# Kernel optimization log

Measured on AMD Instinct MI355X. Metric: run time of the kernel, lower is better.

## Reference

```python
import jax, jax.numpy as jnp
import numpy as np

TEMP = 0.1
NEG = -1e30  # stands in for removing the diagonal via masked_select
EPS = 1e-12  # F.normalize eps


def _l2norm(x, axis):
    n = jnp.linalg.norm(x, axis=axis, keepdims=True)
    return x / jnp.maximum(n, EPS)


def setup_inputs() -> dict:
    key = jax.random.key(0)
    k = jax.random.split(key, 6)
    B, D = 8192, 128      # instance batch, embed dim
    Bp, P = 256, 256      # patch batch, patches per sample
    v1_ins = jax.random.normal(k[0], (B, D), jnp.float32)
    v2_ins = jax.random.normal(k[1], (B, D), jnp.float32)
    v1_patch = jax.random.normal(k[2], (Bp, D, P), jnp.float32)
    v2_patch = jax.random.normal(k[3], (Bp, D, P), jnp.float32)
    v1_counts = jax.random.randint(k[4], (Bp, P), 0, 50, dtype=jnp.int32)
    v2_counts = jax.random.randint(k[5], (Bp, P), 0, 50, dtype=jnp.int32)
    return {"v1_ins": v1_ins, "v2_ins": v2_ins,
            "v1_patch": v1_patch, "v2_patch": v2_patch,
            "v1_counts": v1_counts, "v2_counts": v2_counts}


def _instance_ce(v1, v2):
    B = v1.shape[0]
    embs = jnp.concatenate([_l2norm(v1, 1), _l2norm(v2, 1)], axis=0)  # [2B, D]
    logits = (embs @ embs.T) / TEMP                                    # [2B, 2B]
    N = 2 * B
    # masking the diagonal to -inf == masked_select removal; positive of row i
    # is column (i+B) mod 2B (matches labels after diagonal removal shift)
    logits = jnp.where(jnp.eye(N, dtype=bool), NEG, logits)
    labels = jnp.concatenate([jnp.arange(B) + B, jnp.arange(B)])
    logp = jax.nn.log_softmax(logits, axis=1)
    return -jnp.mean(logp[jnp.arange(N), labels])


def _patch_ce(v1, v2, c1, c2):
    Bp, D, P = v1.shape
    embs = jnp.concatenate([_l2norm(v1, 1), _l2norm(v2, 1)], axis=2)   # [Bp, D, 2P]
    logits = jnp.einsum('bdi,bdj->bij', embs, embs) / TEMP             # [Bp, 2P, 2P]
    N = 2 * P
    logits = jnp.where(jnp.eye(N, dtype=bool)[None], NEG, logits)
    labels = jnp.concatenate([jnp.arange(P) + P, jnp.arange(P)])       # [2P]
    valid = ~jnp.concatenate([c1 == 0, c2 == 0], axis=1)               # [Bp, 2P]
    logp = jax.nn.log_softmax(logits, axis=2)
    pos = logp[:, jnp.arange(N), labels]                               # [Bp, 2P]
    # ignore_index=-100 -> mean over non-ignored elements
    n_valid = jnp.sum(valid.astype(logits.dtype))
    return -jnp.sum(jnp.where(valid, pos, 0.0)) / n_valid


def reference(v1_ins, v2_ins, v1_patch, v2_patch, v1_counts, v2_counts):
    ins_ce = _instance_ce(v1_ins, v2_ins)
    patch_ce = _patch_ce(v1_patch, v2_patch, v1_counts, v2_counts)
    return ins_ce + patch_ce
```

## Files before the change

kernel.cpp:

```cpp
#include <hip/hip_runtime.h>
#include <math.h>

typedef __bf16 bf16_t;
typedef __bf16 bf16x8 __attribute__((ext_vector_type(8)));
typedef float f32x4 __attribute__((ext_vector_type(4)));
typedef float f32x2 __attribute__((ext_vector_type(2)));

#define B_INS 8192
#define N_INS 16384
#define D 128
#define BP 256
#define P 256
#define NP 512

#define C1_CONST 14.426950408889634f

#define WS_ACC 0
#define WS_POS 8
#define WS_PPOS (WS_POS + N_INS)
#define NPAIRI 8128
#define WS_CI (WS_PPOS + BP * NP)
#define WS_RI (WS_CI + NPAIRI * 256)
#define WS_CP (WS_RI + 1088 * 256)
#define WS_RP (WS_CP + BP * 6 * 256)
#define WS_END (WS_RP + 1024 * 256)
#define EMB_I_BYTE ((((WS_END) * 4 + 15) / 16) * 16)
#define EMB_P_BYTE (EMB_I_BYTE + N_INS * D * 2)


#define NB_NORMI 128
#define NB_NORMP 2048
#define NB_PREP (NB_NORMI + NB_NORMP + 1)
#define NB_INS 1088
#define NB_PATCHB 1024
#define NB_GRAM (NB_INS + NB_PATCHB)
#define NB_FIN (128 + 256)

__device__ __forceinline__ void load_lds16(const bf16_t* g, bf16_t* l) {
    __builtin_amdgcn_global_load_lds(
        (const __attribute__((address_space(1))) void*)g,
        (__attribute__((address_space(3))) void*)l, 16, 0, 0);
}

__device__ __forceinline__ void stage_panel(const bf16_t* __restrict__ src,
                                            bf16_t* dst, int w, int lane) {
    const bf16_t* g = src + w * 4096 + lane * 8;
    bf16_t* d = dst + w * 4096;
#pragma unroll
    for (int it = 0; it < 8; it++)
        load_lds16(g + it * 512, d + it * 512);
}

__device__ __forceinline__ void load_afrags(const bf16_t* __restrict__ abase,
                                            int rh, int tx, int q, bf16x8 af[4][4]) {
    const bf16_t* a = abase + ((rh * 64 + tx) << 3);
#pragma unroll
    for (int rt = 0; rt < 4; rt++)
#pragma unroll
        for (int ks = 0; ks < 4; ks++)
            af[rt][ks] = *(const bf16x8*)(a + (((ks << 2) + q) << 10) + (rt << 7));
}

__global__ __launch_bounds__(256) void prep_k(const float* __restrict__ v1i,
                                              const float* __restrict__ v2i,
                                              const float* __restrict__ v1p,
                                              const float* __restrict__ v2p,
                                              bf16_t* __restrict__ embI,
                                              bf16_t* __restrict__ embP,
                                              float* __restrict__ ws) {
    __shared__ float L[128][65];
    __shared__ float ps[4][64];
    __shared__ float invs[128];
    int bx = blockIdx.x;
    int t = threadIdx.x;
    if (bx < NB_NORMI) {
        int p = bx;
        const float* srcP = (p < 64) ? (v1i + (size_t)p * 128 * D)
                                     : (v2i + (size_t)(p - 64) * 128 * D);
        {
            int r = t >> 1, h = t & 1;
            const float* row = srcP + (size_t)r * D + h * 64;
            float ss = 0.f;
#pragma unroll
            for (int j = 0; j < 16; j++) {
                float4 v = *(const float4*)(row + j * 4);
                ss += v.x * v.x + v.y * v.y + v.z * v.z + v.w * v.w;
            }
            ss += __shfl_xor(ss, 1, 64);
            if (h == 0) invs[r] = 1.0f / fmaxf(sqrtf(ss), 1e-12f);
        }
        __syncthreads();
#pragma unroll
        for (int it = 0; it < 8; it++) {
            int idx = it * 256 + t;
            int r = idx & 127, g = idx >> 7;
            const float* src8 = srcP + (size_t)r * D + g * 8;
            float4 a = *(const float4*)(src8);
            float4 b = *(const float4*)(src8 + 4);
            float inv = invs[r];
            bf16x8 v;
            v[0] = (bf16_t)(a.x * inv); v[1] = (bf16_t)(a.y * inv);
            v[2] = (bf16_t)(a.z * inv); v[3] = (bf16_t)(a.w * inv);
            v[4] = (bf16_t)(b.x * inv); v[5] = (bf16_t)(b.y * inv);
            v[6] = (bf16_t)(b.z * inv); v[7] = (bf16_t)(b.w * inv);
            *(bf16x8*)(embI + ((size_t)p << 14) + (g << 10) + (r << 3)) = v;
        }
    } else if (bx < NB_NORMI + NB_NORMP) {
        int bx2 = bx - NB_NORMI;
        int b = bx2 >> 3, h = (bx2 >> 2) & 1, chunk = bx2 & 3;
        int i0 = chunk * 64;
        const float* src = ((h == 0) ? v1p : v2p) + (size_t)b * D * P;
#pragma unroll
        for (int it = 0; it < 8; it++) {
            int fi = it * 256 + t;
            int d = fi >> 4, c4 = fi & 15;
            float4 v = *(const float4*)(src + (size_t)d * P + i0 + c4 * 4);
            L[d][c4 * 4 + 0] = v.x;
            L[d][c4 * 4 + 1] = v.y;
            L[d][c4 * 4 + 2] = v.z;
            L[d][c4 * 4 + 3] = v.w;
        }
        __syncthreads();
        {
            int col = t & 63, part = t >> 6;
            float ss = 0.f;
#pragma unroll 8
            for (int d = part * 32; d < part * 32 + 32; d++) { float x = L[d][col]; ss += x * x; }
            ps[part][col] = ss;
        }
        __syncthreads();
        if (t < 64) {
            float n2 = ps[0][t] + ps[1][t] + ps[2][t] + ps[3][t];
            invs[t] = 1.0f / fmaxf(sqrtf(n2), 1e-12f);
        }
        __syncthreads();
#pragma unroll
        for (int it = 0; it < 4; it++) {
            int idx = it * 256 + t;
            int ic = idx & 63, g = idx >> 6;
            float inv = invs[ic];
            bf16x8 v;
#pragma unroll
            for (int j = 0; j < 8; j++) v[j] = (bf16_t)(L[g * 8 + j][ic] * inv);
            int iLoc = h * P + i0 + ic;
            *(bf16x8*)(embP + ((size_t)b << 16) + ((size_t)(iLoc >> 7) << 14) +
                       (g << 10) + ((iLoc & 127) << 3)) = v;
        }
    } else {
        if (t < 8) ws[t] = 0.f;
    }
}

__global__ __launch_bounds__(256) void gram_k(const bf16_t* __restrict__ embI,
                                              const bf16_t* __restrict__ embP,
                                              float* __restrict__ pos,
                                              float* __restrict__ posp,
                                              float* __restrict__ colI,
                                              float* __restrict__ rowI,
                                              float* __restrict__ colP,
                                              float* __restrict__ rowP) {
    __shared__ __align__(16) bf16_t shB[2][16384];
    int t = threadIdx.x, w = t >> 6, lane = t & 63;
    int tx = lane & 15, q = lane >> 4;
    int rh = w & 1, ch = w >> 1;
    int bx = blockIdx.x;

    const bf16_t *Abase, *Bbase;
    float *posArr, *colArr, *rowDst;
    int R, c0, n, diagC, posC;
    if (bx < NB_INS) {
        int bid = bx, k = 0, cum = 0;
        while (bid >= cum + 8 * (16 - k)) { cum += 8 * (16 - k); k++; }
        int rem = bid - cum, cc = 16 - k;
        R = 8 * k + rem / cc;
        int ci = rem - (rem / cc) * cc;
        c0 = R + ci * 8;
        n = min(8, 128 - c0);
        Abase = embI + ((size_t)R << 14);
        Bbase = embI;
        posArr = pos;
        colArr = colI + (size_t)R * 256;
        rowDst = rowI + (size_t)(R * 16 + ci) * 256;
        diagC = R; posC = R + 64;
    } else {
        int pi = bx - NB_INS;
        int b = pi >> 2; R = pi & 3;
        c0 = R; n = 4 - R;
        const bf16_t* base = embP + ((size_t)b << 16);
        Abase = base + ((size_t)R << 14);
        Bbase = base;
        posArr = posp + (size_t)b * NP;
        colArr = colP + (size_t)(b * 6 + R) * 256;
        rowDst = rowP + (size_t)((b << 2) + R) * 256;
        diagC = R; posC = R + 2;
    }
    int rowBase = R * 128;

    bf16x8 af[4][4];
    load_afrags(Abase, rh, tx, q, af);

    f32x2 rowS2[8];
#pragma unroll
    for (int i = 0; i < 8; i++) rowS2[i] = (f32x2){0.f, 0.f};

    stage_panel(Bbase + ((size_t)c0 << 14), shB[0], w, lane);
    int cur = 0;
    for (int ti = 0; ti < n; ti++) {
        int C = c0 + ti;
        __syncthreads();
        if (ti + 1 < n)
            stage_panel(Bbase + ((size_t)(C + 1) << 14), shB[cur ^ 1], w, lane);
        bool isDiag = (C == diagC), isPos = (C == posC);
        int colBase = C * 128;
        const bf16_t* sb = shB[cur];

        float colS[4];
#pragma unroll
        for (int nt = 0; nt < 4; nt++) {
            bf16x8 bf[4];
#pragma unroll
            for (int ks = 0; ks < 4; ks++)
                bf[ks] = *(const bf16x8*)(sb + (((ks << 2) + q) << 10) +
                                          ((ch * 64 + nt * 16 + tx) << 3));
            f32x4 acc[4];
#pragma unroll
            for (int rt = 0; rt < 4; rt++) acc[rt] = (f32x4){0.f, 0.f, 0.f, 0.f};
            __builtin_amdgcn_s_setprio(1);
#pragma unroll
            for (int ks = 0; ks < 4; ks++)
#pragma unroll
                for (int rt = 0; rt < 4; rt++)
                    acc[rt] = __builtin_amdgcn_mfma_f32_16x16x32_bf16(
                        af[rt][ks], bf[ks], acc[rt], 0, 0, 0);
            __builtin_amdgcn_s_setprio(0);

            f32x2 cs = (f32x2){0.f, 0.f};
#pragma unroll
            for (int rt = 0; rt < 4; rt++) {
                f32x2 l0 = {acc[rt][0], acc[rt][1]};
                f32x2 l1 = {acc[rt][2], acc[rt][3]};
                l0 = l0 * C1_CONST - C1_CONST;
                l1 = l1 * C1_CONST - C1_CONST;
                f32x2 e0 = {__builtin_amdgcn_exp2f(l0.x), __builtin_amdgcn_exp2f(l0.y)};
                f32x2 e1 = {__builtin_amdgcn_exp2f(l1.x), __builtin_amdgcn_exp2f(l1.y)};
                if (isDiag) {
                    int inRow = rh * 64 + rt * 16 + q * 4;
                    int inCol = ch * 64 + nt * 16 + tx;
                    if (inRow + 0 == inCol) e0.x = 0.f;
                    if (inRow + 1 == inCol) e0.y = 0.f;
                    if (inRow + 2 == inCol) e1.x = 0.f;
                    if (inRow + 3 == inCol) e1.y = 0.f;
                }
                rowS2[rt * 2] += e0;
                rowS2[rt * 2 + 1] += e1;
                cs += e0 + e1;
            }
            colS[nt] = cs.x + cs.y;

            if (isPos && ch == rh) {
                int reg = tx - q * 4;
                if (reg >= 0 && reg < 4) {
                    float pl = acc[nt][reg] * 10.0f;
                    posArr[rowBase + rh * 64 + nt * 16 + tx] = pl;
                    posArr[colBase + rh * 64 + nt * 16 + tx] = pl;
                }
            }
        }
        if (!isDiag) {
#pragma unroll
            for (int i = 0; i < 4; i++) {
                colS[i] += __shfl_xor(colS[i], 16, 64);
                colS[i] += __shfl_xor(colS[i], 32, 64);
            }
            if (q == 0) {
                float* cdst = colArr + (size_t)(C * (C - 1) / 2) * 256 + rh * 128;
#pragma unroll
                for (int nt = 0; nt < 4; nt++)
                    cdst[ch * 64 + nt * 16 + tx] = colS[nt];
            }
        }
        cur ^= 1;
    }
    float* rowS = (float*)rowS2;
#pragma unroll
    for (int off = 1; off <= 8; off <<= 1)
#pragma unroll
        for (int i = 0; i < 16; i++) rowS[i] += __shfl_xor(rowS[i], off, 16);
    if (tx == 0) {
#pragma unroll
        for (int rt = 0; rt < 4; rt++)
#pragma unroll
            for (int reg = 0; reg < 4; reg++)
                rowDst[ch * 128 + rh * 64 + rt * 16 + q * 4 + reg] =
                    rowS[rt * 4 + reg];
    }
}

__global__ __launch_bounds__(512) void fin_k(const float* __restrict__ pos,
                                             const float* __restrict__ posp,
                                             const float* __restrict__ colI,
                                             const float* __restrict__ rowI,
                                             const float* __restrict__ colP,
                                             const float* __restrict__ rowP,
                                             const int* __restrict__ c1,
                                             const int* __restrict__ c2,
                                             float* __restrict__ acc,
                                             float* __restrict__ out) {
    int bx = blockIdx.x, t = threadIdx.x;
    int lane = t & 63, w = t >> 6;
    float va = 0.f, nv = 0.f;
    __shared__ float part[2][2][128];
    if (bx < 128) {
        int p = 127 - bx;
        int u = t >> 8, half = (t >> 7) & 1, r = t & 127;
        int cc = 16 - (p >> 3);
        float s0 = 0.f, s1 = 0.f, s2 = 0.f, s3 = 0.f;
        const float* RIp = rowI + (size_t)(p * 16) * 256 + half * 128 + r;
        int ci = u;
        for (; ci + 6 < cc; ci += 8) {
            s0 += RIp[ci * 256];       s1 += RIp[(ci + 2) * 256];
            s2 += RIp[(ci + 4) * 256]; s3 += RIp[(ci + 6) * 256];
        }
        for (; ci < cc; ci += 2) s0 += RIp[ci * 256];
        const float* CIp = colI + (size_t)(p * (p - 1) / 2) * 256 + half * 128 + r;
        int Rq = u;
        for (; Rq + 6 < p; Rq += 8) {
            s0 += CIp[Rq * 256];       s1 += CIp[(Rq + 2) * 256];
            s2 += CIp[(Rq + 4) * 256]; s3 += CIp[(Rq + 6) * 256];
        }
        for (; Rq < p; Rq += 2) s0 += CIp[Rq * 256];
        part[u][half][r] = (s0 + s1) + (s2 + s3);
        __syncthreads();
        if (t < 128) {
            float S = (part[0][0][t] + part[0][1][t]) +
                      (part[1][0][t] + part[1][1][t]);
            va = __logf(S) + 10.0f - pos[p * 128 + t];
        }
    } else {
        int b = bx - 128;
        int idx = t;
        int p = idx >> 7, r = idx & 127;
        const float* RPp = rowP + (size_t)((b << 2) + p) * 256 + r;
        float s = RPp[0] + RPp[128];
        const float* CPp = colP + (size_t)(b * 6 + p * (p - 1) / 2) * 256 + r;
        for (int Rq = 0; Rq < p; Rq++) s += CPp[Rq * 256] + CPp[Rq * 256 + 128];
        int cnt = (idx < P) ? c1[b * P + idx] : c2[b * P + idx - P];
        if (cnt != 0) {
            va = __logf(s) + 10.0f - posp[b * NP + idx];
            nv = 1.0f;
        }
    }
#pragma unroll
    for (int off = 32; off >= 1; off >>= 1) {
        va += __shfl_down(va, off, 64);
        nv += __shfl_down(nv, off, 64);
    }
    __shared__ float psum[8], pn[8];
    if (lane == 0) { psum[w] = va; pn[w] = nv; }
    __syncthreads();
    if (t == 0) {
        float sv = 0.f, sn = 0.f;
#pragma unroll
        for (int i = 0; i < 8; i++) { sv += psum[i]; sn += pn[i]; }
        if (bx < 128) {
            atomicAdd(&acc[0], sv);
        } else {
            atomicAdd(&acc[1], sv);
            atomicAdd(&acc[2], sn);
        }
        __threadfence();
        unsigned old = atomicAdd((unsigned*)&acc[3], 1u);
        if (old == NB_FIN - 1) {
            float a0 = atomicAdd(&acc[0], 0.0f);
            float a1 = atomicAdd(&acc[1], 0.0f);
            float a2 = atomicAdd(&acc[2], 0.0f);
            out[0] = a0 * (1.0f / (float)N_INS) + a1 / a2;
        }
    }
}

extern "C" void kernel_launch(void* const* d_in, const int* in_sizes, int n_in,
                              void* d_out, int out_size, void* d_ws, size_t ws_size,
                              hipStream_t stream) {
    const float* v1i = (const float*)d_in[0];
    const float* v2i = (const float*)d_in[1];
    const float* v1p = (const float*)d_in[2];
    const float* v2p = (const float*)d_in[3];
    const int* c1 = (const int*)d_in[4];
    const int* c2 = (const int*)d_in[5];
    float* ws = (float*)d_ws;
    float* out = (float*)d_out;
    bf16_t* embI = (bf16_t*)((char*)d_ws + EMB_I_BYTE);
    bf16_t* embP = (bf16_t*)((char*)d_ws + EMB_P_BYTE);

    prep_k<<<NB_PREP, 256, 0, stream>>>(v1i, v2i, v1p, v2p, embI, embP, ws);
    gram_k<<<NB_GRAM, 256, 0, stream>>>(embI, embP, ws + WS_POS, ws + WS_PPOS,
                                        ws + WS_CI, ws + WS_RI,
                                        ws + WS_CP, ws + WS_RP);
    fin_k<<<NB_FIN, 512, 0, stream>>>(ws + WS_POS, ws + WS_PPOS, ws + WS_CI,
                                      ws + WS_RI, ws + WS_CP, ws + WS_RP,
                                      c1, c2, ws + WS_ACC, out);
}
```

Measured before the change: 205.8 us.

## Interleave MFMA tiles with exp epilogue and fold logit scale into normalization

The instance and patch norm factors are now scaled by sqrt(C1), so the bf16 embeddings give dot products already multiplied by 1/(T·ln2). The accumulators start at -C1 instead of zero. This removes the per-element scale-and-shift FMA before exp2, and the positive logit is recovered as (acc+C1)·ln2. The four column sub-tiles are also processed ping-pong with two accumulator and B-fragment sets, so the MFMAs of one sub-tile are issued before the exp/reduction epilogue of the previous one, overlapping matrix and vector work. This costs more live VGPRs, which could lower occupancy or cause spills.

```diff
diff --git a/kernel.cpp b/kernel.cpp
--- a/kernel.cpp
+++ b/kernel.cpp
@@ -14,6 +14,8 @@
 #define NP 512
 
 #define C1_CONST 14.426950408889634f
+#define SQRT_C1 3.798283f
+#define LN2_CONST 0.69314718056f
 
 #define WS_ACC 0
 #define WS_POS 8
@@ -87,7 +89,7 @@
                 ss += v.x * v.x + v.y * v.y + v.z * v.z + v.w * v.w;
             }
             ss += __shfl_xor(ss, 1, 64);
-            if (h == 0) invs[r] = 1.0f / fmaxf(sqrtf(ss), 1e-12f);
+            if (h == 0) invs[r] = SQRT_C1 / fmaxf(sqrtf(ss), 1e-12f);
         }
         __syncthreads();
 #pragma unroll
@@ -131,7 +133,7 @@
         __syncthreads();
         if (t < 64) {
             float n2 = ps[0][t] + ps[1][t] + ps[2][t] + ps[3][t];
-            invs[t] = 1.0f / fmaxf(sqrtf(n2), 1e-12f);
+            invs[t] = SQRT_C1 / fmaxf(sqrtf(n2), 1e-12f);
         }
         __syncthreads();
 #pragma unroll
@@ -203,6 +205,50 @@
 #pragma unroll
     for (int i = 0; i < 8; i++) rowS2[i] = (f32x2){0.f, 0.f};
 
+#define LOADBF(BF, NT)                                                        \
+    _Pragma("unroll") for (int ks = 0; ks < 4; ks++)                          \
+        BF[ks] = *(const bf16x8*)(sb + (((ks << 2) + q) << 10) +              \
+                                  ((ch * 64 + (NT) * 16 + tx) << 3));
+
+#define MFMAS(ACC, BF)                                                        \
+    _Pragma("unroll") for (int rt = 0; rt < 4; rt++)                          \
+        ACC[rt] = (f32x4){-C1_CONST, -C1_CONST, -C1_CONST, -C1_CONST};        \
+    __builtin_amdgcn_s_setprio(1);                                            \
+    _Pragma("unroll") for (int ks = 0; ks < 4; ks++)                          \
+        _Pragma("unroll") for (int rt = 0; rt < 4; rt++)                      \
+            ACC[rt] = __builtin_amdgcn_mfma_f32_16x16x32_bf16(                \
+                af[rt][ks], BF[ks], ACC[rt], 0, 0, 0);                        \
+    __builtin_amdgcn_s_setprio(0);
+
+#define EPI(NT, ACC) {                                                        \
+    f32x2 cs = (f32x2){0.f, 0.f};                                             \
+    _Pragma("unroll") for (int rt = 0; rt < 4; rt++) {                        \
+        f32x2 e0 = {__builtin_amdgcn_exp2f(ACC[rt][0]),                       \
+                    __builtin_amdgcn_exp2f(ACC[rt][1])};                      \
+        f32x2 e1 = {__builtin_amdgcn_exp2f(ACC[rt][2]),                       \
+                    __builtin_amdgcn_exp2f(ACC[rt][3])};                      \
+        if (isDiag) {                                                         \
+            int inRow = rh * 64 + rt * 16 + q * 4;                            \
+            int inCol = ch * 64 + (NT) * 16 + tx;                             \
+            if (inRow + 0 == inCol) e0.x = 0.f;                               \
+            if (inRow + 1 == inCol) e0.y = 0.f;                               \
+            if (inRow + 2 == inCol) e1.x = 0.f;                               \
+            if (inRow + 3 == inCol) e1.y = 0.f;                               \
+        }                                                                     \
+        rowS2[rt * 2] += e0;                                                  \
+        rowS2[rt * 2 + 1] += e1;                                              \
+        cs += e0 + e1;                                                        \
+    }                                                                         \
+    colS[NT] = cs.x + cs.y;                                                   \
+    if (isPos && ch == rh) {                                                  \
+        int reg = tx - q * 4;                                                 \
+        if (reg >= 0 && reg < 4) {                                            \
+            float pl = (ACC[NT][reg] + C1_CONST) * LN2_CONST;                 \
+            posArr[rowBase + rh * 64 + (NT) * 16 + tx] = pl;                  \
+            posArr[colBase + rh * 64 + (NT) * 16 + tx] = pl;                  \
+        }                                                                     \
+    } }
+
     stage_panel(Bbase + ((size_t)c0 << 14), shB[0], w, lane);
     int cur = 0;
     for (int ti = 0; ti < n; ti++) {
@@ -215,57 +261,17 @@
         const bf16_t* sb = shB[cur];
 
         float colS[4];
-#pragma unroll
-        for (int nt = 0; nt < 4; nt++) {
-            bf16x8 bf[4];
-#pragma unroll
-            for (int ks = 0; ks < 4; ks++)
-                bf[ks] = *(const bf16x8*)(sb + (((ks << 2) + q) << 10) +
-                                          ((ch * 64 + nt * 16 + tx) << 3));
-            f32x4 acc[4];
-#pragma unroll
-            for (int rt = 0; rt < 4; rt++) acc[rt] = (f32x4){0.f, 0.f, 0.f, 0.f};
-            __builtin_amdgcn_s_setprio(1);
-#pragma unroll
-            for (int ks = 0; ks < 4; ks++)
-#pragma unroll
-                for (int rt = 0; rt < 4; rt++)
-                    acc[rt] = __builtin_amdgcn_mfma_f32_16x16x32_bf16(
-                        af[rt][ks], bf[ks], acc[rt], 0, 0, 0);
-            __builtin_amdgcn_s_setprio(0);
-
-            f32x2 cs = (f32x2){0.f, 0.f};
-#pragma unroll
-            for (int rt = 0; rt < 4; rt++) {
-                f32x2 l0 = {acc[rt][0], acc[rt][1]};
-                f32x2 l1 = {acc[rt][2], acc[rt][3]};
-                l0 = l0 * C1_CONST - C1_CONST;
-                l1 = l1 * C1_CONST - C1_CONST;
-                f32x2 e0 = {__builtin_amdgcn_exp2f(l0.x), __builtin_amdgcn_exp2f(l0.y)};
-                f32x2 e1 = {__builtin_amdgcn_exp2f(l1.x), __builtin_amdgcn_exp2f(l1.y)};
-                if (isDiag) {
-                    int inRow = rh * 64 + rt * 16 + q * 4;
-                    int inCol = ch * 64 + nt * 16 + tx;
-                    if (inRow + 0 == inCol) e0.x = 0.f;
-                    if (inRow + 1 == inCol) e0.y = 0.f;
-                    if (inRow + 2 == inCol) e1.x = 0.f;
-                    if (inRow + 3 == inCol) e1.y = 0.f;
-                }
-                rowS2[rt * 2] += e0;
-                rowS2[rt * 2 + 1] += e1;
-                cs += e0 + e1;
-            }
-            colS[nt] = cs.x + cs.y;
-
-            if (isPos && ch == rh) {
-                int reg = tx - q * 4;
-                if (reg >= 0 && reg < 4) {
-                    float pl = acc[nt][reg] * 10.0f;
-                    posArr[rowBase + rh * 64 + nt * 16 + tx] = pl;
-                    posArr[colBase + rh * 64 + nt * 16 + tx] = pl;
-                }
-            }
-        }
+        bf16x8 bfA[4], bfB[4];
+        f32x4 accA[4], accB[4];
+        LOADBF(bfA, 0) MFMAS(accA, bfA)
+        LOADBF(bfB, 1) MFMAS(accB, bfB)
+        EPI(0, accA)
+        LOADBF(bfA, 2) MFMAS(accA, bfA)
+        EPI(1, accB)
+        LOADBF(bfB, 3) MFMAS(accB, bfB)
+        EPI(2, accA)
+        EPI(3, accB)
+
         if (!isDiag) {
 #pragma unroll
             for (int i = 0; i < 4; i++) {
@@ -294,6 +300,9 @@
                 rowDst[ch * 128 + rh * 64 + rt * 16 + q * 4 + reg] =
                     rowS[rt * 4 + reg];
     }
+#undef LOADBF
+#undef MFMAS
+#undef EPI
 }
 
 __global__ __launch_bounds__(512) void fin_k(const float* __restrict__ pos,
```

Result: no change. 203.3 us, median of 2 (-1.3%).
